# Performance work log

Hardware: AMD Instinct MI355X
Metric: run time of the kernel (lower is better)

## Reference

```python
import jax, jax.numpy as jnp
import numpy as np

B, S, N, C, D = 1, 6, 10000, 128, 4
HEADS, PTS = 4, 8
HF, WF = 28, 50
M = HF * WF


def setup_inputs() -> dict:
    key0 = jax.random.key(0)
    ks = jax.random.split(key0, 14)
    sc = C ** -0.5
    d = {}
    d["query"] = jax.random.normal(ks[0], (B, N, C), jnp.float32)
    d["key"] = jax.random.normal(ks[1], (S, M, B, C), jnp.float32)
    d["value"] = jax.random.normal(ks[2], (S, M, B, C), jnp.float32)
    d["query_pos"] = jax.random.normal(ks[3], (B, N, C), jnp.float32) * 0.1
    d["reference_points_cam"] = jax.random.uniform(ks[4], (S, B, N, D, 2), jnp.float32, -0.2, 1.2)
    d["bev_mask"] = jax.random.randint(ks[5], (S, B, N, D), 0, 2).astype(bool)
    d["w_off"] = jax.random.normal(ks[6], (C, HEADS * PTS * 2), jnp.float32) * sc
    d["b_off"] = jax.random.normal(ks[7], (HEADS * PTS * 2,), jnp.float32) * 0.01
    d["w_attn"] = jax.random.normal(ks[8], (C, HEADS * PTS), jnp.float32) * sc
    d["b_attn"] = jax.random.normal(ks[9], (HEADS * PTS,), jnp.float32) * 0.01
    d["w_val"] = jax.random.normal(ks[10], (C, C), jnp.float32) * sc
    d["b_val"] = jax.random.normal(ks[11], (C,), jnp.float32) * 0.01
    d["w_out"] = jax.random.normal(ks[12], (C, C), jnp.float32) * sc
    d["b_out"] = jax.random.normal(ks[13], (C,), jnp.float32) * 0.01
    d["Hf"] = HF
    d["Wf"] = WF
    return d


def reference(query, key, value, query_pos, reference_points_cam, bev_mask,
              w_off, b_off, w_attn, b_attn, w_val, b_val, w_out, b_out, Hf, Wf):
    # SpatialCrossAttention with MSDeformAttn3D (BEVFormer semantics, eval mode: dropout=identity).
    # The torch data-dependent gather/rebatch/scatter is replaced by mathematically equivalent
    # masked computation: deformable attention is per-query independent, so running it for all
    # BEV queries per camera and mask-accumulating yields identical slots.
    B_, N_, C_ = query.shape
    S_ = key.shape[0]
    D_ = reference_points_cam.shape[3]
    H, P = HEADS, PTS
    dh = C_ // H
    Pd = P // D_
    q = query + query_pos  # (B,N,C)
    off = (q @ w_off + b_off).reshape(B_, N_, H, Pd, D_, 2)
    aw = jax.nn.softmax((q @ w_attn + b_attn).reshape(B_, N_, H, P), axis=-1)  # over levels*points (L=1)
    # value projection; per-camera feature maps laid out as (B,S,H,Hf*Wf,dh)
    v = jnp.transpose(value, (2, 0, 1, 3))  # (B,S,M,C)
    v = v @ w_val + b_val
    v = v.reshape(B_, S_, Hf * Wf, H, dh).transpose(0, 1, 3, 2, 4)  # (B,S,H,M,dh)
    ref = jnp.transpose(reference_points_cam, (1, 0, 2, 3, 4))  # (B,S,N,D,2)
    norm = jnp.array([Wf, Hf], jnp.float32)  # offset_normalizer = (W, H)
    loc = ref[:, :, :, None, None, :, :] + off[:, None] / norm  # (B,S,N,H,Pd,D,2)
    loc = loc.reshape(B_, S_, N_, H, P, 2)
    # bilinear sampling, zero padding, align_corners=False
    ix = loc[..., 0] * Wf - 0.5
    iy = loc[..., 1] * Hf - 0.5
    x0 = jnp.floor(ix)
    y0 = jnp.floor(iy)

    def flat(a):  # (B,S,N,H,P) -> (B,S,H,N*P)
        return a.transpose(0, 1, 3, 2, 4).reshape(B_, S_, H, N_ * P)

    def gather(xi, yi):
        ok = (xi >= 0) & (xi < Wf) & (yi >= 0) & (yi < Hf)
        xi_c = jnp.clip(xi, 0, Wf - 1).astype(jnp.int32)
        yi_c = jnp.clip(yi, 0, Hf - 1).astype(jnp.int32)
        idx = flat(yi_c * Wf + xi_c)
        g = jnp.take_along_axis(v, idx[..., None], axis=3)  # (B,S,H,N*P,dh)
        return g * flat(ok.astype(v.dtype))[..., None]

    wx1 = ix - x0
    wy1 = iy - y0
    wx0 = 1.0 - wx1
    wy0 = 1.0 - wy1
    samp = (gather(x0, y0) * flat(wx0 * wy0)[..., None]
            + gather(x0 + 1, y0) * flat(wx1 * wy0)[..., None]
            + gather(x0, y0 + 1) * flat(wx0 * wy1)[..., None]
            + gather(x0 + 1, y0 + 1) * flat(wx1 * wy1)[..., None])  # (B,S,H,N*P,dh)
    samp = samp.reshape(B_, S_, H, N_, P, dh)
    out = jnp.einsum('bshnpd,bnhp->bsnhd', samp, aw).reshape(B_, S_, N_, C_)
    # masked scatter-accumulate back to BEV slots
    mask = jnp.transpose(jnp.any(bev_mask, axis=-1), (1, 0, 2))  # (B,S,N)
    slots = jnp.sum(out * mask[..., None].astype(out.dtype), axis=1)  # (B,N,C)
    count = jnp.maximum(mask.astype(out.dtype).sum(axis=1), 1.0)
    slots = slots / count[..., None]
    return slots @ w_out + b_out + query  # dropout is identity in eval
```

## Files before the change

### kernel.cpp

```cpp
#include <hip/hip_runtime.h>
#include <math.h>

#define S_ 6
#define N_ 10000
#define C_ 128
#define D_ 4
#define H_ 4
#define P_ 8
#define HF_ 28
#define WF_ 50
#define M_ (HF_ * WF_)
#define DH_ 32
#define SM_ (S_ * M_)
#define QB_ 8
#define ABYTES (S_ * H_ * M_ * 32)

#define NB_V ((SM_ + 31) / 32)
#define NB_O ((N_ + 31) / 32)

typedef float floatx2 __attribute__((ext_vector_type(2)));
typedef _Float16 half4h __attribute__((ext_vector_type(4)));

template <int NC, int MT, int MR, int MODE>
__device__ __forceinline__ void gemm_body(
    const float* __restrict__ A, const float* __restrict__ A2,
    const float* __restrict__ B0, const float* __restrict__ B1,
    const float* __restrict__ bias0, const float* __restrict__ bias1,
    float* __restrict__ outf, char* __restrict__ out8,
    int Mrows, int m0, int tid, int nthreads, float (*Alds)[132]) {
  constexpr int NTHR = (NC / 4) * (MT / MR);

  for (int i = tid; i < MT * 32; i += nthreads) {
    int r = i >> 5, k = (i & 31) * 4;
    int row = m0 + r;
    float4 v = make_float4(0.f, 0.f, 0.f, 0.f);
    if (row < Mrows) {
      v = *(const float4*)(A + (size_t)row * C_ + k);
      if (MODE == 1) {
        float4 v2 = *(const float4*)(A2 + (size_t)row * C_ + k);
        v.x += v2.x; v.y += v2.y; v.z += v2.z; v.w += v2.w;
      }
    }
    *(float4*)(&Alds[r][k]) = v;
  }
  __syncthreads();
  if (tid >= NTHR) return;

  int ci = tid % (NC / 4);
  int mi = tid / (NC / 4);
  int c0 = ci * 4, r0 = mi * MR;

  const float* bs;
  if (MODE == 1) bs = (c0 < 64) ? bias0 + c0 : bias1 + (c0 - 64);
  else bs = bias0 + c0;

  float acc[MR][4];
#pragma unroll
  for (int j = 0; j < MR; ++j)
#pragma unroll
    for (int cc = 0; cc < 4; ++cc) acc[j][cc] = bs[cc];

#pragma unroll 2
  for (int k4 = 0; k4 < C_; k4 += 4) {
    float bf[16];
#pragma unroll
    for (int kk = 0; kk < 4; ++kk) {
      int k = k4 + kk;
      float4 b4;
      if (MODE == 1)
        b4 = (c0 < 64) ? *(const float4*)(B0 + (size_t)k * 64 + c0)
                       : *(const float4*)(B1 + (size_t)k * 32 + (c0 - 64));
      else
        b4 = *(const float4*)(B0 + (size_t)k * NC + c0);
      bf[kk * 4 + 0] = b4.x; bf[kk * 4 + 1] = b4.y;
      bf[kk * 4 + 2] = b4.z; bf[kk * 4 + 3] = b4.w;
    }
    float af[MR * 4];
#pragma unroll
    for (int j = 0; j < MR; ++j) {
      float4 a4 = *(const float4*)(&Alds[r0 + j][k4]);
      af[j * 4 + 0] = a4.x; af[j * 4 + 1] = a4.y;
      af[j * 4 + 2] = a4.z; af[j * 4 + 3] = a4.w;
    }
#pragma unroll
    for (int j = 0; j < MR; ++j)
#pragma unroll
      for (int kk = 0; kk < 4; ++kk)
#pragma unroll
        for (int cc = 0; cc < 4; ++cc)
          acc[j][cc] = fmaf(af[j * 4 + kk], bf[kk * 4 + cc], acc[j][cc]);
  }

#pragma unroll
  for (int j = 0; j < MR; ++j) {
    int row = m0 + r0 + j;
    if (row >= Mrows) continue;
    if (MODE == 0) {
      int s = row / M_, mm = row % M_;
      int y = mm / WF_, x = mm % WF_;
      int h = c0 >> 5, d0 = c0 & 31;
      int w = __builtin_amdgcn_cvt_pk_fp8_f32(acc[j][0], acc[j][1], 0, false);
      w = __builtin_amdgcn_cvt_pk_fp8_f32(acc[j][2], acc[j][3], w, true);
      size_t hm = (size_t)s * H_ + h;
      *(int*)(out8 + (hm * M_ + mm) * 32 + d0) = w;
      if (x > 0) {
        int kp = (x - 1) >> 1, slot = 1 - (x & 1);
        *(int*)(out8 + ABYTES + ((hm * HF_ + y) * 25 + kp) * 64 +
                slot * 32 + d0) = w;
      }
    } else if (MODE == 1) {
      *(float4*)(outf + (size_t)row * 96 + c0) =
          make_float4(acc[j][0], acc[j][1], acc[j][2], acc[j][3]);
    }
  }
}

__global__ __launch_bounds__(256) void prep_kernel(
    const float* __restrict__ value, const float* __restrict__ w_val,
    const float* __restrict__ b_val, char* __restrict__ vh8,
    const float* __restrict__ query, const float* __restrict__ query_pos,
    const float* __restrict__ w_off, const float* __restrict__ b_off,
    const float* __restrict__ w_attn, const float* __restrict__ b_attn,
    float* __restrict__ OFFL) {
  __shared__ float Alds[32][132];
  int bid = blockIdx.x;
  if (bid < NB_V) {
    gemm_body<128, 32, 4, 0>(value, nullptr, w_val, nullptr, b_val, nullptr,
                             nullptr, vh8, SM_, bid * 32, threadIdx.x, 256,
                             Alds);
  } else {
    gemm_body<96, 32, 4, 1>(query, query_pos, w_off, w_attn, b_off, b_attn,
                            OFFL, nullptr, N_, (bid - NB_V) * 32, threadIdx.x,
                            256, Alds);
  }
}

__global__ __launch_bounds__(256) void attn2_kernel(
    const float* __restrict__ OFFL,
    const float* __restrict__ refpts,
    const int*   __restrict__ bev_mask,
    const char*  __restrict__ wsbase,
    const float* __restrict__ query,
    const float* __restrict__ w_out,
    const float* __restrict__ b_out,
    float* __restrict__ out) {
  int n0 = blockIdx.x * QB_;
  int tid = threadIdx.x;

  __shared__ char smem[30656];
  int2*   sidx  = (int2*)smem;
  half4h* swh   = (half4h*)(smem + 12416);
  float*  offp  = (float*)(smem + 24832);
  float*  logtp = (float*)(smem + 24832 + 2048);
  float*  awp   = (float*)(smem + 24832 + 3072);
  float*  reflp = (float*)(smem + 24832 + 4096);
  float*  slp   = (float*)(smem + 24832);
  int*    smaskp= (int*)(smem + 30464);

  for (int i = tid; i < QB_ * 96; i += 256) {
    int q = i / 96, c = i % 96;
    float v = OFFL[(size_t)(n0 + q) * 96 + c];
    if (c < 64) offp[q * 64 + c] = v; else logtp[q * 32 + c - 64] = v;
  }
  for (int i = tid; i < QB_ * 48; i += 256) {
    int q = i / 48, rem = i % 48;
    int s = rem >> 3, r8 = rem & 7;
    reflp[q * 48 + rem] = refpts[((size_t)s * N_ + (n0 + q)) * 8 + r8];
  }
  if (tid < QB_ * 6) {
    int q = tid / 6, s = tid % 6;
    const int* bm = bev_mask + ((size_t)s * N_ + (n0 + q)) * D_;
    smaskp[tid] = (bm[0] | bm[1] | bm[2] | bm[3]) ? 1 : 0;
  }
  __syncthreads();

  {
    int q = tid >> 5, j = tid & 31, h = j >> 3;
    float mx = -1e30f;
#pragma unroll
    for (int p = 0; p < P_; ++p) mx = fmaxf(mx, logtp[q * 32 + h * P_ + p]);
    float sum = 0.f;
#pragma unroll
    for (int p = 0; p < P_; ++p) sum += expf(logtp[q * 32 + h * P_ + p] - mx);
    awp[q * 32 + j] = expf(logtp[q * 32 + j] - mx) / sum;
  }
  __syncthreads();

  for (int i = tid; i < QB_ * 192; i += 256) {
    int q = i / 192, j = i % 192;
    int s = j >> 5, w32 = j & 31, p = w32 >> 2, h = w32 & 3;
    int pd = p >> 2, dd = p & 3;
    float rx = reflp[q * 48 + s * 8 + dd * 2 + 0];
    float ry = reflp[q * 48 + s * 8 + dd * 2 + 1];
    float ox = offp[q * 64 + h * 16 + pd * 8 + dd * 2 + 0];
    float oy = offp[q * 64 + h * 16 + pd * 8 + dd * 2 + 1];
    float ix = rx * (float)WF_ + ox - 0.5f;
    float iy = ry * (float)HF_ + oy - 0.5f;
    float x0f = floorf(ix), y0f = floorf(iy);
    int x0 = (int)x0f, y0 = (int)y0f;
    float wx1 = ix - x0f, wy1 = iy - y0f;
    float wx0 = 1.f - wx1, wy0 = 1.f - wy1;
    float a = awp[q * 32 + h * P_ + p] * (float)smaskp[q * 6 + s];
    bool vx0 = (x0 >= 0) && (x0 < WF_);
    bool vx1 = (x0 + 1 >= 0) && (x0 + 1 < WF_);
    bool vy0 = (y0 >= 0) && (y0 < HF_);
    bool vy1 = (y0 + 1 >= 0) && (y0 + 1 < HF_);
    int y0c = min(max(y0, 0), HF_ - 1);
    int y1c = min(max(y0 + 1, 0), HF_ - 1);
    int hm = s * H_ + h;
    int itop, ibot;
    if (x0 >= 0 && x0 <= WF_ - 2 && !(x0 & 1)) {
      itop = (hm * M_ + y0c * WF_ + x0) * 32;
      ibot = (hm * M_ + y1c * WF_ + x0) * 32;
    } else if (x0 >= 1 && x0 <= WF_ - 1 && (x0 & 1)) {
      int kp = (x0 - 1) >> 1;
      itop = ABYTES + ((hm * HF_ + y0c) * 25 + kp) * 64;
      ibot = ABYTES + ((hm * HF_ + y1c) * 25 + kp) * 64;
    } else if (x0 == -1) {
      itop = (hm * M_ + y0c * WF_) * 32 - 32;
      ibot = (hm * M_ + y1c * WF_) * 32 - 32;
    } else {
      itop = ibot = 0;
    }
    float w00 = (vx0 && vy0) ? wx0 * wy0 * a : 0.f;
    float w10 = (vx1 && vy0) ? wx1 * wy0 * a : 0.f;
    float w01 = (vx0 && vy1) ? wx0 * wy1 * a : 0.f;
    float w11 = (vx1 && vy1) ? wx1 * wy1 * a : 0.f;
    sidx[q * 194 + j] = make_int2(itop + 64, ibot + 64);
    half4h wv = {(_Float16)w00, (_Float16)w10, (_Float16)w01, (_Float16)w11};
    swh[q * 194 + j] = wv;
  }
  __syncthreads();

  {
    int q = tid >> 5, t = tid & 31, h = t >> 3, c8 = t & 7;
    int rowsel = (c8 >> 2) & 1;
    int xsel   = (c8 >> 1) & 1;
    int chalf  = c8 & 1;
    int role   = c8 >> 1;
    int lanebyte = xsel * 32 + chalf * 16;
    const int* sxi = (const int*)(sidx + q * 194);
    const _Float16* swq = (const _Float16*)(swh + q * 194);

    int offR[48];
    _Float16 wR[48];
#pragma unroll
    for (int u = 0; u < 48; ++u) {
      int j = (u >> 3) * 32 + (u & 7) * 4 + h;
      offR[u] = sxi[j * 2 + rowsel];
      wR[u] = swq[j * 4 + role];
    }

    floatx2 acc[8] = {{0.f, 0.f}, {0.f, 0.f}, {0.f, 0.f}, {0.f, 0.f},
                      {0.f, 0.f}, {0.f, 0.f}, {0.f, 0.f}, {0.f, 0.f}};
#pragma unroll
    for (int u = 0; u < 48; ++u) {
      float w = (float)wR[u];
      floatx2 wv = {w, w};
      int4 tq = *(const int4*)(wsbase + (offR[u] + lanebyte));
      acc[0] += __builtin_amdgcn_cvt_pk_f32_fp8(tq.x, false) * wv;
      acc[1] += __builtin_amdgcn_cvt_pk_f32_fp8(tq.x, true)  * wv;
      acc[2] += __builtin_amdgcn_cvt_pk_f32_fp8(tq.y, false) * wv;
      acc[3] += __builtin_amdgcn_cvt_pk_f32_fp8(tq.y, true)  * wv;
      acc[4] += __builtin_amdgcn_cvt_pk_f32_fp8(tq.z, false) * wv;
      acc[5] += __builtin_amdgcn_cvt_pk_f32_fp8(tq.z, true)  * wv;
      acc[6] += __builtin_amdgcn_cvt_pk_f32_fp8(tq.w, false) * wv;
      acc[7] += __builtin_amdgcn_cvt_pk_f32_fp8(tq.w, true)  * wv;
    }
    float av[16];
#pragma unroll
    for (int k = 0; k < 8; ++k) { av[2 * k] = acc[k][0]; av[2 * k + 1] = acc[k][1]; }
#pragma unroll
    for (int k = 0; k < 16; ++k) av[k] += __shfl_xor(av[k], 2);
#pragma unroll
    for (int k = 0; k < 16; ++k) av[k] += __shfl_xor(av[k], 4);

    int cnt = smaskp[q * 6 + 0] + smaskp[q * 6 + 1] + smaskp[q * 6 + 2] +
              smaskp[q * 6 + 3] + smaskp[q * 6 + 4] + smaskp[q * 6 + 5];
    float inv = 1.f / (float)(cnt > 0 ? cnt : 1);
    if (c8 < 2) {
      float* dst = &slp[q * 132 + h * DH_ + chalf * 16];
#pragma unroll
      for (int k = 0; k < 16; ++k) dst[k] = av[k] * inv;
    }
  }
  __syncthreads();

  {
    int q2 = tid >> 5, c0 = (tid & 31) * 4;
    int n = n0 + q2;
    float4 qv = *(const float4*)(query + (size_t)n * C_ + c0);
    float4 bv = *(const float4*)(b_out + c0);
    floatx2 r01 = {bv.x + qv.x, bv.y + qv.y};
    floatx2 r23 = {bv.z + qv.z, bv.w + qv.w};
#pragma unroll 4
    for (int k = 0; k < C_; ++k) {
      floatx2 a = {slp[q2 * 132 + k], slp[q2 * 132 + k]};
      float4 w4 = *(const float4*)(w_out + (size_t)k * C_ + c0);
      floatx2 w01 = {w4.x, w4.y}, w23 = {w4.z, w4.w};
      r01 += a * w01;
      r23 += a * w23;
    }
    *(float4*)(out + (size_t)n * C_ + c0) =
        make_float4(r01[0], r01[1], r23[0], r23[1]);
  }
}

extern "C" void kernel_launch(void* const* d_in, const int* in_sizes, int n_in,
                              void* d_out, int out_size, void* d_ws, size_t ws_size,
                              hipStream_t stream) {
  const float* query     = (const float*)d_in[0];
  const float* value     = (const float*)d_in[2];
  const float* query_pos = (const float*)d_in[3];
  const float* refpts    = (const float*)d_in[4];
  const int*   bev_mask  = (const int*)d_in[5];
  const float* w_off     = (const float*)d_in[6];
  const float* b_off     = (const float*)d_in[7];
  const float* w_attn    = (const float*)d_in[8];
  const float* b_attn    = (const float*)d_in[9];
  const float* w_val     = (const float*)d_in[10];
  const float* b_val     = (const float*)d_in[11];
  const float* w_out     = (const float*)d_in[12];
  const float* b_out     = (const float*)d_in[13];

  char* ws = (char*)d_ws;
  char* vh8   = ws + 64;
  float* OFFL = (float*)(ws + 64 + 2 * (size_t)ABYTES + 64);

  prep_kernel<<<NB_V + NB_O, 256, 0, stream>>>(
      value, w_val, b_val, vh8, query, query_pos, w_off, b_off, w_attn, b_attn,
      OFFL);
  attn2_kernel<<<N_ / QB_, 256, 0, stream>>>(OFFL, refpts, bev_mask, ws,
                                             query, w_out, b_out,
                                             (float*)d_out);
}
```

Measured before the change: 151.2 us.

## Halve queries per block and split sampling and output GEMM across wave halves

Reduces queries per attention block from 8 to 4, doubling the grid, and gives each query a full 64-lane wave. The two half-waves split the six cameras during bilinear sampling and the K dimension in the output projection, then combine partial sums with a cross-half shuffle. The aim is more blocks in flight and shorter per-thread gather chains to hide memory latency. In exchange, the index and weight setup and the w_out reads are repeated across twice as many blocks, and extra shuffles are added.

```diff
diff --git a/kernel.cpp b/kernel.cpp
--- a/kernel.cpp
+++ b/kernel.cpp
@@ -12,7 +12,7 @@
 #define M_ (HF_ * WF_)
 #define DH_ 32
 #define SM_ (S_ * M_)
-#define QB_ 8
+#define QB_ 4
 #define ABYTES (S_ * H_ * M_ * 32)
 
 #define NB_V ((SM_ + 31) / 32)
@@ -147,15 +147,14 @@
   int n0 = blockIdx.x * QB_;
   int tid = threadIdx.x;
 
-  __shared__ char smem[30656];
-  int2*   sidx  = (int2*)smem;
-  half4h* swh   = (half4h*)(smem + 12416);
-  float*  offp  = (float*)(smem + 24832);
-  float*  logtp = (float*)(smem + 24832 + 2048);
-  float*  awp   = (float*)(smem + 24832 + 3072);
-  float*  reflp = (float*)(smem + 24832 + 4096);
-  float*  slp   = (float*)(smem + 24832);
-  int*    smaskp= (int*)(smem + 30464);
+  __shared__ int2   sidx[QB_ * 194];
+  __shared__ half4h swh[QB_ * 194];
+  __shared__ float  offp[QB_ * 64];
+  __shared__ float  logtp[QB_ * 32];
+  __shared__ float  awp[QB_ * 32];
+  __shared__ float  reflp[QB_ * 48];
+  __shared__ int    smaskp[QB_ * 6];
+  __shared__ float  slp[QB_ * 132];
 
   for (int i = tid; i < QB_ * 96; i += 256) {
     int q = i / 96, c = i % 96;
@@ -174,7 +173,7 @@
   }
   __syncthreads();
 
-  {
+  if (tid < QB_ * 32) {
     int q = tid >> 5, j = tid & 31, h = j >> 3;
     float mx = -1e30f;
 #pragma unroll
@@ -233,7 +232,9 @@
   __syncthreads();
 
   {
-    int q = tid >> 5, t = tid & 31, h = t >> 3, c8 = t & 7;
+    int q = tid >> 6, lane = tid & 63;
+    int ssel = lane >> 5;
+    int t = lane & 31, h = t >> 3, c8 = t & 7;
     int rowsel = (c8 >> 2) & 1;
     int xsel   = (c8 >> 1) & 1;
     int chalf  = c8 & 1;
@@ -242,11 +243,11 @@
     const int* sxi = (const int*)(sidx + q * 194);
     const _Float16* swq = (const _Float16*)(swh + q * 194);
 
-    int offR[48];
-    _Float16 wR[48];
-#pragma unroll
-    for (int u = 0; u < 48; ++u) {
-      int j = (u >> 3) * 32 + (u & 7) * 4 + h;
+    int offR[24];
+    _Float16 wR[24];
+#pragma unroll
+    for (int u = 0; u < 24; ++u) {
+      int j = (ssel * 3 + (u >> 3)) * 32 + (u & 7) * 4 + h;
       offR[u] = sxi[j * 2 + rowsel];
       wR[u] = swq[j * 4 + role];
     }
@@ -254,7 +255,7 @@
     floatx2 acc[8] = {{0.f, 0.f}, {0.f, 0.f}, {0.f, 0.f}, {0.f, 0.f},
                       {0.f, 0.f}, {0.f, 0.f}, {0.f, 0.f}, {0.f, 0.f}};
 #pragma unroll
-    for (int u = 0; u < 48; ++u) {
+    for (int u = 0; u < 24; ++u) {
       float w = (float)wR[u];
       floatx2 wv = {w, w};
       int4 tq = *(const int4*)(wsbase + (offR[u] + lanebyte));
@@ -274,11 +275,13 @@
     for (int k = 0; k < 16; ++k) av[k] += __shfl_xor(av[k], 2);
 #pragma unroll
     for (int k = 0; k < 16; ++k) av[k] += __shfl_xor(av[k], 4);
+#pragma unroll
+    for (int k = 0; k < 16; ++k) av[k] += __shfl_xor(av[k], 32);
 
     int cnt = smaskp[q * 6 + 0] + smaskp[q * 6 + 1] + smaskp[q * 6 + 2] +
               smaskp[q * 6 + 3] + smaskp[q * 6 + 4] + smaskp[q * 6 + 5];
     float inv = 1.f / (float)(cnt > 0 ? cnt : 1);
-    if (c8 < 2) {
+    if (ssel == 0 && c8 < 2) {
       float* dst = &slp[q * 132 + h * DH_ + chalf * 16];
 #pragma unroll
       for (int k = 0; k < 16; ++k) dst[k] = av[k] * inv;
@@ -287,22 +290,33 @@
   __syncthreads();
 
   {
-    int q2 = tid >> 5, c0 = (tid & 31) * 4;
+    int q2 = tid >> 6, lane = tid & 63;
+    int khalf = lane >> 5;
+    int c0 = (lane & 31) * 4;
     int n = n0 + q2;
-    float4 qv = *(const float4*)(query + (size_t)n * C_ + c0);
-    float4 bv = *(const float4*)(b_out + c0);
-    floatx2 r01 = {bv.x + qv.x, bv.y + qv.y};
-    floatx2 r23 = {bv.z + qv.z, bv.w + qv.w};
+    floatx2 r01 = {0.f, 0.f};
+    floatx2 r23 = {0.f, 0.f};
+    int k0 = khalf * 64;
 #pragma unroll 4
-    for (int k = 0; k < C_; ++k) {
+    for (int kk = 0; kk < 64; ++kk) {
+      int k = k0 + kk;
       floatx2 a = {slp[q2 * 132 + k], slp[q2 * 132 + k]};
       float4 w4 = *(const float4*)(w_out + (size_t)k * C_ + c0);
       floatx2 w01 = {w4.x, w4.y}, w23 = {w4.z, w4.w};
       r01 += a * w01;
       r23 += a * w23;
     }
-    *(float4*)(out + (size_t)n * C_ + c0) =
-        make_float4(r01[0], r01[1], r23[0], r23[1]);
+    r01[0] += __shfl_xor(r01[0], 32);
+    r01[1] += __shfl_xor(r01[1], 32);
+    r23[0] += __shfl_xor(r23[0], 32);
+    r23[1] += __shfl_xor(r23[1], 32);
+    if (lane < 32) {
+      float4 qv = *(const float4*)(query + (size_t)n * C_ + c0);
+      float4 bv = *(const float4*)(b_out + c0);
+      *(float4*)(out + (size_t)n * C_ + c0) =
+          make_float4(r01[0] + bv.x + qv.x, r01[1] + bv.y + qv.y,
+                      r23[0] + bv.z + qv.z, r23[1] + bv.w + qv.w);
+    }
   }
 }
 
```

Result: no change. 150.2 us (-0.7%).

## Stage per-camera-head value maps in LDS and split attention into partial-sum plus reduce

Applied to the files above, without the earlier changes.

The attention kernel is reorganized so each block owns one (camera, head) pair and a chunk of 256 queries. It copies that pair's fp8 value map (about 45 KB) into LDS and does the bilinear taps from shared memory instead of scattered global loads. This drops the duplicate shifted value layout from the prep kernel. Per-head partial results go to a global buffer, and a new reduce kernel sums over cameras, normalizes by mask count and applies the output projection with a register-tiled GEMM. The cost is an extra kernel launch, a partial-sum round trip through global memory, and every block reloading a full value map.

```diff
diff --git a/kernel.cpp b/kernel.cpp
--- a/kernel.cpp
+++ b/kernel.cpp
@@ -12,14 +12,17 @@
 #define M_ (HF_ * WF_)
 #define DH_ 32
 #define SM_ (S_ * M_)
-#define QB_ 8
 #define ABYTES (S_ * H_ * M_ * 32)
+#define VB_SH (M_ * 32)
+#define NSH (S_ * H_)
+#define CQ 256
+#define NCH ((N_ + CQ - 1) / CQ)
 
 #define NB_V ((SM_ + 31) / 32)
 #define NB_O ((N_ + 31) / 32)
 
 typedef float floatx2 __attribute__((ext_vector_type(2)));
-typedef _Float16 half4h __attribute__((ext_vector_type(4)));
+typedef _Float16 half2h __attribute__((ext_vector_type(2)));
 
 template <int NC, int MT, int MR, int MODE>
 __device__ __forceinline__ void gemm_body(
@@ -96,18 +99,13 @@
     int row = m0 + r0 + j;
     if (row >= Mrows) continue;
     if (MODE == 0) {
-      int s = row / M_, mm = row % M_;
-      int y = mm / WF_, x = mm % WF_;
+      int mm = row % M_;
       int h = c0 >> 5, d0 = c0 & 31;
+      int s = row / M_;
       int w = __builtin_amdgcn_cvt_pk_fp8_f32(acc[j][0], acc[j][1], 0, false);
       w = __builtin_amdgcn_cvt_pk_fp8_f32(acc[j][2], acc[j][3], w, true);
       size_t hm = (size_t)s * H_ + h;
       *(int*)(out8 + (hm * M_ + mm) * 32 + d0) = w;
-      if (x > 0) {
-        int kp = (x - 1) >> 1, slot = 1 - (x & 1);
-        *(int*)(out8 + ABYTES + ((hm * HF_ + y) * 25 + kp) * 64 +
-                slot * 32 + d0) = w;
-      }
     } else if (MODE == 1) {
       *(float4*)(outf + (size_t)row * 96 + c0) =
           make_float4(acc[j][0], acc[j][1], acc[j][2], acc[j][3]);
@@ -135,174 +133,234 @@
   }
 }
 
-__global__ __launch_bounds__(256) void attn2_kernel(
+__global__ __launch_bounds__(256, 2) void attn3_kernel(
     const float* __restrict__ OFFL,
     const float* __restrict__ refpts,
     const int*   __restrict__ bev_mask,
     const char*  __restrict__ wsbase,
-    const float* __restrict__ query,
-    const float* __restrict__ w_out,
-    const float* __restrict__ b_out,
-    float* __restrict__ out) {
-  int n0 = blockIdx.x * QB_;
+    float* __restrict__ part) {
+  __shared__ int4 Vl4[VB_SH / 16];
+  __shared__ int4 Pp[CQ * 9];
+
+  int bid = blockIdx.x;
+  int sh = bid % NSH;
+  int q0 = (bid / NSH) * CQ;
+  int s = sh >> 2, h = sh & 3;
   int tid = threadIdx.x;
 
-  __shared__ char smem[30656];
-  int2*   sidx  = (int2*)smem;
-  half4h* swh   = (half4h*)(smem + 12416);
-  float*  offp  = (float*)(smem + 24832);
-  float*  logtp = (float*)(smem + 24832 + 2048);
-  float*  awp   = (float*)(smem + 24832 + 3072);
-  float*  reflp = (float*)(smem + 24832 + 4096);
-  float*  slp   = (float*)(smem + 24832);
-  int*    smaskp= (int*)(smem + 30464);
-
-  for (int i = tid; i < QB_ * 96; i += 256) {
-    int q = i / 96, c = i % 96;
-    float v = OFFL[(size_t)(n0 + q) * 96 + c];
-    if (c < 64) offp[q * 64 + c] = v; else logtp[q * 32 + c - 64] = v;
-  }
-  for (int i = tid; i < QB_ * 48; i += 256) {
-    int q = i / 48, rem = i % 48;
-    int s = rem >> 3, r8 = rem & 7;
-    reflp[q * 48 + rem] = refpts[((size_t)s * N_ + (n0 + q)) * 8 + r8];
-  }
-  if (tid < QB_ * 6) {
-    int q = tid / 6, s = tid % 6;
-    const int* bm = bev_mask + ((size_t)s * N_ + (n0 + q)) * D_;
-    smaskp[tid] = (bm[0] | bm[1] | bm[2] | bm[3]) ? 1 : 0;
+  const int4* vsrc = (const int4*)(wsbase + 64 + (size_t)sh * VB_SH);
+#pragma unroll 4
+  for (int i = tid; i < VB_SH / 16; i += 256) Vl4[i] = vsrc[i];
+
+  {
+    int q = q0 + tid;
+    float aw[8], rx[4], ry[4];
+    int sm = 0;
+    if (q < N_) {
+      const float* lg = OFFL + (size_t)q * 96 + 64 + h * 8;
+      float mx = -1e30f;
+#pragma unroll
+      for (int p = 0; p < 8; ++p) mx = fmaxf(mx, lg[p]);
+      float sum = 0.f;
+#pragma unroll
+      for (int p = 0; p < 8; ++p) { aw[p] = expf(lg[p] - mx); sum += aw[p]; }
+      float is = 1.f / sum;
+#pragma unroll
+      for (int p = 0; p < 8; ++p) aw[p] *= is;
+      const int* bm = bev_mask + ((size_t)s * N_ + q) * D_;
+      sm = (bm[0] | bm[1] | bm[2] | bm[3]) ? 1 : 0;
+      const float* rf = refpts + ((size_t)s * N_ + q) * 8;
+#pragma unroll
+      for (int dd = 0; dd < 4; ++dd) {
+        rx[dd] = rf[dd * 2 + 0];
+        ry[dd] = rf[dd * 2 + 1];
+      }
+    }
+#pragma unroll
+    for (int p = 0; p < 8; ++p) {
+      int4 pk = {0, 0, 0, 0};
+      if (q < N_) {
+        int pd = p >> 2, dd = p & 3;
+        float ox = OFFL[(size_t)q * 96 + h * 16 + pd * 8 + dd * 2 + 0];
+        float oy = OFFL[(size_t)q * 96 + h * 16 + pd * 8 + dd * 2 + 1];
+        float ix = rx[dd] * (float)WF_ + ox - 0.5f;
+        float iy = ry[dd] * (float)HF_ + oy - 0.5f;
+        float xf = floorf(ix), yf = floorf(iy);
+        int x0 = (int)xf, y0 = (int)yf;
+        float wx1 = ix - xf, wy1 = iy - yf;
+        float wx0 = 1.f - wx1, wy0 = 1.f - wy1;
+        float a = aw[p] * (float)sm;
+        bool vx0 = (x0 >= 0) && (x0 < WF_);
+        bool vx1 = (x0 + 1 >= 0) && (x0 + 1 < WF_);
+        bool vy0 = (y0 >= 0) && (y0 < HF_);
+        bool vy1 = (y0 + 1 >= 0) && (y0 + 1 < HF_);
+        float w00 = (vx0 && vy0) ? wx0 * wy0 * a : 0.f;
+        float w10 = (vx1 && vy0) ? wx1 * wy0 * a : 0.f;
+        float w01 = (vx0 && vy1) ? wx0 * wy1 * a : 0.f;
+        float w11 = (vx1 && vy1) ? wx1 * wy1 * a : 0.f;
+        int yt = min(max(y0, 0), HF_ - 1) * WF_;
+        int yb = min(max(y0 + 1, 0), HF_ - 1) * WF_;
+        int xc0 = min(max(x0, 0), WF_ - 1);
+        int xc1 = min(max(x0 + 1, 0), WF_ - 1);
+        pk.x = yt | (yb << 16);
+        pk.y = xc0 | (xc1 << 16);
+        union { half2h hv; int iv; } u01, u23;
+        u01.hv = (half2h){(_Float16)w00, (_Float16)w10};
+        u23.hv = (half2h){(_Float16)w01, (_Float16)w11};
+        pk.z = u01.iv;
+        pk.w = u23.iv;
+      }
+      Pp[tid * 9 + p] = pk;
+    }
   }
   __syncthreads();
 
   {
-    int q = tid >> 5, j = tid & 31, h = j >> 3;
-    float mx = -1e30f;
-#pragma unroll
-    for (int p = 0; p < P_; ++p) mx = fmaxf(mx, logtp[q * 32 + h * P_ + p]);
-    float sum = 0.f;
-#pragma unroll
-    for (int p = 0; p < P_; ++p) sum += expf(logtp[q * 32 + h * P_ + p] - mx);
-    awp[q * 32 + j] = expf(logtp[q * 32 + j] - mx) / sum;
+    int w = tid >> 6, lane = tid & 63;
+    int qg = lane >> 3, c8 = lane & 7;
+    int rowsel = (c8 >> 2) & 1, xsel = (c8 >> 1) & 1, chalf = c8 & 1;
+    int role = c8 >> 1;
+    int rsh = rowsel << 4, xsh = xsel << 4, wsh = (role & 1) << 4;
+
+    for (int pass = 0; pass < CQ / 32; ++pass) {
+      int ql = pass * 32 + w * 8 + qg;
+      int q = q0 + ql;
+      const int4* pp = &Pp[ql * 9];
+      floatx2 acc[8] = {{0.f, 0.f}, {0.f, 0.f}, {0.f, 0.f}, {0.f, 0.f},
+                        {0.f, 0.f}, {0.f, 0.f}, {0.f, 0.f}, {0.f, 0.f}};
+#pragma unroll
+      for (int p = 0; p < 8; ++p) {
+        int4 prm = pp[p];
+        int yoff = (prm.x >> rsh) & 0xffff;
+        int xoff = (prm.y >> xsh) & 0xffff;
+        int vidx = (yoff + xoff) * 2 + chalf;
+        unsigned wz = (unsigned)((role & 2) ? prm.w : prm.z);
+        union { unsigned short u; _Float16 hf; } cu;
+        cu.u = (unsigned short)((wz >> wsh) & 0xffffu);
+        float wgt = (float)cu.hf;
+        floatx2 wv = {wgt, wgt};
+        int4 tv = Vl4[vidx];
+        acc[0] += __builtin_amdgcn_cvt_pk_f32_fp8(tv.x, false) * wv;
+        acc[1] += __builtin_amdgcn_cvt_pk_f32_fp8(tv.x, true)  * wv;
+        acc[2] += __builtin_amdgcn_cvt_pk_f32_fp8(tv.y, false) * wv;
+        acc[3] += __builtin_amdgcn_cvt_pk_f32_fp8(tv.y, true)  * wv;
+        acc[4] += __builtin_amdgcn_cvt_pk_f32_fp8(tv.z, false) * wv;
+        acc[5] += __builtin_amdgcn_cvt_pk_f32_fp8(tv.z, true)  * wv;
+        acc[6] += __builtin_amdgcn_cvt_pk_f32_fp8(tv.w, false) * wv;
+        acc[7] += __builtin_amdgcn_cvt_pk_f32_fp8(tv.w, true)  * wv;
+      }
+      float av[16];
+#pragma unroll
+      for (int k = 0; k < 8; ++k) {
+        av[2 * k] = acc[k][0];
+        av[2 * k + 1] = acc[k][1];
+      }
+#pragma unroll
+      for (int k = 0; k < 16; ++k) av[k] += __shfl_xor(av[k], 2);
+#pragma unroll
+      for (int k = 0; k < 16; ++k) av[k] += __shfl_xor(av[k], 4);
+      if (c8 < 2 && q < N_) {
+        float* dst = part + ((size_t)sh * N_ + q) * 32 + chalf * 16;
+        *(float4*)(dst + 0)  = make_float4(av[0], av[1], av[2], av[3]);
+        *(float4*)(dst + 4)  = make_float4(av[4], av[5], av[6], av[7]);
+        *(float4*)(dst + 8)  = make_float4(av[8], av[9], av[10], av[11]);
+        *(float4*)(dst + 12) = make_float4(av[12], av[13], av[14], av[15]);
+      }
+    }
+  }
+}
+
+__global__ __launch_bounds__(256) void reduce_kernel(
+    const float* __restrict__ part, const int* __restrict__ bev_mask,
+    const float* __restrict__ query, const float* __restrict__ w_out,
+    const float* __restrict__ b_out, float* __restrict__ out) {
+  __shared__ float slds[32][132];
+  __shared__ float sinv[32];
+  int q0 = blockIdx.x * 32, tid = threadIdx.x;
+
+  if (tid < 32) {
+    int q = q0 + tid, cnt = 0;
+    if (q < N_) {
+#pragma unroll
+      for (int s = 0; s < S_; ++s) {
+        const int* bm = bev_mask + ((size_t)s * N_ + q) * D_;
+        cnt += (bm[0] | bm[1] | bm[2] | bm[3]) ? 1 : 0;
+      }
+    }
+    sinv[tid] = 1.f / (float)(cnt > 0 ? cnt : 1);
   }
   __syncthreads();
 
-  for (int i = tid; i < QB_ * 192; i += 256) {
-    int q = i / 192, j = i % 192;
-    int s = j >> 5, w32 = j & 31, p = w32 >> 2, h = w32 & 3;
-    int pd = p >> 2, dd = p & 3;
-    float rx = reflp[q * 48 + s * 8 + dd * 2 + 0];
-    float ry = reflp[q * 48 + s * 8 + dd * 2 + 1];
-    float ox = offp[q * 64 + h * 16 + pd * 8 + dd * 2 + 0];
-    float oy = offp[q * 64 + h * 16 + pd * 8 + dd * 2 + 1];
-    float ix = rx * (float)WF_ + ox - 0.5f;
-    float iy = ry * (float)HF_ + oy - 0.5f;
-    float x0f = floorf(ix), y0f = floorf(iy);
-    int x0 = (int)x0f, y0 = (int)y0f;
-    float wx1 = ix - x0f, wy1 = iy - y0f;
-    float wx0 = 1.f - wx1, wy0 = 1.f - wy1;
-    float a = awp[q * 32 + h * P_ + p] * (float)smaskp[q * 6 + s];
-    bool vx0 = (x0 >= 0) && (x0 < WF_);
-    bool vx1 = (x0 + 1 >= 0) && (x0 + 1 < WF_);
-    bool vy0 = (y0 >= 0) && (y0 < HF_);
-    bool vy1 = (y0 + 1 >= 0) && (y0 + 1 < HF_);
-    int y0c = min(max(y0, 0), HF_ - 1);
-    int y1c = min(max(y0 + 1, 0), HF_ - 1);
-    int hm = s * H_ + h;
-    int itop, ibot;
-    if (x0 >= 0 && x0 <= WF_ - 2 && !(x0 & 1)) {
-      itop = (hm * M_ + y0c * WF_ + x0) * 32;
-      ibot = (hm * M_ + y1c * WF_ + x0) * 32;
-    } else if (x0 >= 1 && x0 <= WF_ - 1 && (x0 & 1)) {
-      int kp = (x0 - 1) >> 1;
-      itop = ABYTES + ((hm * HF_ + y0c) * 25 + kp) * 64;
-      ibot = ABYTES + ((hm * HF_ + y1c) * 25 + kp) * 64;
-    } else if (x0 == -1) {
-      itop = (hm * M_ + y0c * WF_) * 32 - 32;
-      ibot = (hm * M_ + y1c * WF_) * 32 - 32;
-    } else {
-      itop = ibot = 0;
-    }
-    float w00 = (vx0 && vy0) ? wx0 * wy0 * a : 0.f;
-    float w10 = (vx1 && vy0) ? wx1 * wy0 * a : 0.f;
-    float w01 = (vx0 && vy1) ? wx0 * wy1 * a : 0.f;
-    float w11 = (vx1 && vy1) ? wx1 * wy1 * a : 0.f;
-    sidx[q * 194 + j] = make_int2(itop + 64, ibot + 64);
-    half4h wv = {(_Float16)w00, (_Float16)w10, (_Float16)w01, (_Float16)w11};
-    swh[q * 194 + j] = wv;
+  {
+    int ql = tid >> 3, c16 = (tid & 7) * 16;
+    int q = q0 + ql, h = c16 >> 5, d0 = c16 & 31;
+    float a[16];
+#pragma unroll
+    for (int k = 0; k < 16; ++k) a[k] = 0.f;
+    if (q < N_) {
+#pragma unroll
+      for (int s = 0; s < S_; ++s) {
+        const float* src = part + ((size_t)(s * H_ + h) * N_ + q) * 32 + d0;
+#pragma unroll
+        for (int k = 0; k < 16; k += 4) {
+          float4 v = *(const float4*)(src + k);
+          a[k + 0] += v.x; a[k + 1] += v.y; a[k + 2] += v.z; a[k + 3] += v.w;
+        }
+      }
+    }
+    float inv = sinv[ql];
+    float* dst = &slds[ql][c16];
+#pragma unroll
+    for (int k = 0; k < 16; k += 4)
+      *(float4*)(dst + k) =
+          make_float4(a[k] * inv, a[k + 1] * inv, a[k + 2] * inv, a[k + 3] * inv);
   }
   __syncthreads();
 
   {
-    int q = tid >> 5, t = tid & 31, h = t >> 3, c8 = t & 7;
-    int rowsel = (c8 >> 2) & 1;
-    int xsel   = (c8 >> 1) & 1;
-    int chalf  = c8 & 1;
-    int role   = c8 >> 1;
-    int lanebyte = xsel * 32 + chalf * 16;
-    const int* sxi = (const int*)(sidx + q * 194);
-    const _Float16* swq = (const _Float16*)(swh + q * 194);
-
-    int offR[48];
-    _Float16 wR[48];
-#pragma unroll
-    for (int u = 0; u < 48; ++u) {
-      int j = (u >> 3) * 32 + (u & 7) * 4 + h;
-      offR[u] = sxi[j * 2 + rowsel];
-      wR[u] = swq[j * 4 + role];
-    }
-
-    floatx2 acc[8] = {{0.f, 0.f}, {0.f, 0.f}, {0.f, 0.f}, {0.f, 0.f},
-                      {0.f, 0.f}, {0.f, 0.f}, {0.f, 0.f}, {0.f, 0.f}};
-#pragma unroll
-    for (int u = 0; u < 48; ++u) {
-      float w = (float)wR[u];
-      floatx2 wv = {w, w};
-      int4 tq = *(const int4*)(wsbase + (offR[u] + lanebyte));
-      acc[0] += __builtin_amdgcn_cvt_pk_f32_fp8(tq.x, false) * wv;
-      acc[1] += __builtin_amdgcn_cvt_pk_f32_fp8(tq.x, true)  * wv;
-      acc[2] += __builtin_amdgcn_cvt_pk_f32_fp8(tq.y, false) * wv;
-      acc[3] += __builtin_amdgcn_cvt_pk_f32_fp8(tq.y, true)  * wv;
-      acc[4] += __builtin_amdgcn_cvt_pk_f32_fp8(tq.z, false) * wv;
-      acc[5] += __builtin_amdgcn_cvt_pk_f32_fp8(tq.z, true)  * wv;
-      acc[6] += __builtin_amdgcn_cvt_pk_f32_fp8(tq.w, false) * wv;
-      acc[7] += __builtin_amdgcn_cvt_pk_f32_fp8(tq.w, true)  * wv;
-    }
-    float av[16];
-#pragma unroll
-    for (int k = 0; k < 8; ++k) { av[2 * k] = acc[k][0]; av[2 * k + 1] = acc[k][1]; }
-#pragma unroll
-    for (int k = 0; k < 16; ++k) av[k] += __shfl_xor(av[k], 2);
-#pragma unroll
-    for (int k = 0; k < 16; ++k) av[k] += __shfl_xor(av[k], 4);
-
-    int cnt = smaskp[q * 6 + 0] + smaskp[q * 6 + 1] + smaskp[q * 6 + 2] +
-              smaskp[q * 6 + 3] + smaskp[q * 6 + 4] + smaskp[q * 6 + 5];
-    float inv = 1.f / (float)(cnt > 0 ? cnt : 1);
-    if (c8 < 2) {
-      float* dst = &slp[q * 132 + h * DH_ + chalf * 16];
-#pragma unroll
-      for (int k = 0; k < 16; ++k) dst[k] = av[k] * inv;
-    }
-  }
-  __syncthreads();
-
-  {
-    int q2 = tid >> 5, c0 = (tid & 31) * 4;
-    int n = n0 + q2;
-    float4 qv = *(const float4*)(query + (size_t)n * C_ + c0);
-    float4 bv = *(const float4*)(b_out + c0);
-    floatx2 r01 = {bv.x + qv.x, bv.y + qv.y};
-    floatx2 r23 = {bv.z + qv.z, bv.w + qv.w};
-#pragma unroll 4
-    for (int k = 0; k < C_; ++k) {
-      floatx2 a = {slp[q2 * 132 + k], slp[q2 * 132 + k]};
-      float4 w4 = *(const float4*)(w_out + (size_t)k * C_ + c0);
-      floatx2 w01 = {w4.x, w4.y}, w23 = {w4.z, w4.w};
-      r01 += a * w01;
-      r23 += a * w23;
-    }
-    *(float4*)(out + (size_t)n * C_ + c0) =
-        make_float4(r01[0], r01[1], r23[0], r23[1]);
+    int ci = tid & 31, mi = tid >> 5;
+    int c0 = ci * 4, r0 = mi * 4;
+    float acc[4][4];
+#pragma unroll
+    for (int j = 0; j < 4; ++j) {
+      int q = q0 + r0 + j;
+      int qq = (q < N_) ? q : (N_ - 1);
+      float4 qv = *(const float4*)(query + (size_t)qq * C_ + c0);
+      float4 bv = *(const float4*)(b_out + c0);
+      acc[j][0] = bv.x + qv.x; acc[j][1] = bv.y + qv.y;
+      acc[j][2] = bv.z + qv.z; acc[j][3] = bv.w + qv.w;
+    }
+#pragma unroll 2
+    for (int k4 = 0; k4 < C_; k4 += 4) {
+      float bf[16];
+#pragma unroll
+      for (int kk = 0; kk < 4; ++kk) {
+        float4 b4 = *(const float4*)(w_out + (size_t)(k4 + kk) * C_ + c0);
+        bf[kk * 4 + 0] = b4.x; bf[kk * 4 + 1] = b4.y;
+        bf[kk * 4 + 2] = b4.z; bf[kk * 4 + 3] = b4.w;
+      }
+      float af[16];
+#pragma unroll
+      for (int j = 0; j < 4; ++j) {
+        float4 a4 = *(const float4*)(&slds[r0 + j][k4]);
+        af[j * 4 + 0] = a4.x; af[j * 4 + 1] = a4.y;
+        af[j * 4 + 2] = a4.z; af[j * 4 + 3] = a4.w;
+      }
+#pragma unroll
+      for (int j = 0; j < 4; ++j)
+#pragma unroll
+        for (int kk = 0; kk < 4; ++kk)
+#pragma unroll
+          for (int cc = 0; cc < 4; ++cc)
+            acc[j][cc] = fmaf(af[j * 4 + kk], bf[kk * 4 + cc], acc[j][cc]);
+    }
+#pragma unroll
+    for (int j = 0; j < 4; ++j) {
+      int q = q0 + r0 + j;
+      if (q < N_)
+        *(float4*)(out + (size_t)q * C_ + c0) =
+            make_float4(acc[j][0], acc[j][1], acc[j][2], acc[j][3]);
+    }
   }
 }
 
@@ -326,11 +384,15 @@
   char* ws = (char*)d_ws;
   char* vh8   = ws + 64;
   float* OFFL = (float*)(ws + 64 + 2 * (size_t)ABYTES + 64);
+  float* PART = (float*)(ws + 64 + 2 * (size_t)ABYTES + 64 +
+                         (size_t)N_ * 96 * 4);
 
   prep_kernel<<<NB_V + NB_O, 256, 0, stream>>>(
       value, w_val, b_val, vh8, query, query_pos, w_off, b_off, w_attn, b_attn,
       OFFL);
-  attn2_kernel<<<N_ / QB_, 256, 0, stream>>>(OFFL, refpts, bev_mask, ws,
-                                             query, w_out, b_out,
-                                             (float*)d_out);
-}
+  attn3_kernel<<<NSH * NCH, 256, 0, stream>>>(OFFL, refpts, bev_mask, ws,
+                                              PART);
+  reduce_kernel<<<(N_ + 31) / 32, 256, 0, stream>>>(PART, bev_mask, query,
+                                                    w_out, b_out,
+                                                    (float*)d_out);
+}
```

Result: slower. 165.6 us (+9.5%).
